# Optimization experiments

Measured on AMD Instinct MI355X. Metric: run time of the kernel, lower is better.

The kernel has to match this reference:

```python
import jax, jax.numpy as jnp
import numpy as np

WINDOW_SIZE = 64
SHIFT_SIZE = WINDOW_SIZE // 2  # shift_windows=True
HEAD_DIM = 64
SCALE = HEAD_DIM ** (-0.5)


def _shift_mask(W):
    # static shift-window mask, computed with numpy (all shapes static)
    img_mask = np.zeros((W,), dtype=np.float32)
    cnt = 0
    for s in (slice(0, -WINDOW_SIZE), slice(-WINDOW_SIZE, -SHIFT_SIZE), slice(-SHIFT_SIZE, None)):
        img_mask[s] = cnt
        cnt += 1
    mw = img_mask.reshape(W // WINDOW_SIZE, WINDOW_SIZE)  # (num_win, ws)
    mask = mw[:, None, :] - mw[:, :, None]                # (num_win, ws, ws)
    mask = np.where(mask != 0.0, -100.0, 0.0).astype(np.float32)
    return jnp.asarray(mask)


def setup_inputs() -> dict:
    key = jax.random.key(0)
    k1, k2, k3, k4 = jax.random.split(key, 4)
    B, W, C = 32, 8192, HEAD_DIM
    return {
        "q": jax.random.normal(k1, (B, W, C), dtype=jnp.float32),
        "k": jax.random.normal(k2, (B, W, C), dtype=jnp.float32),
        "v": jax.random.normal(k3, (B, W, C), dtype=jnp.float32),
        "rel_pos_table": jax.random.normal(k4, (2 * WINDOW_SIZE - 1, 1), dtype=jnp.float32) * 0.02,
    }


def reference(q, k, v, rel_pos_table):
    B, W, C = q.shape
    ws = WINDOW_SIZE
    # relative position bias gather: (1, ws, ws)
    coords = jnp.arange(ws)
    rel_idx = coords[None, :] * 0 + (coords[:, None] - coords[None, :]) + (ws - 1)  # (ws, ws)
    bias = rel_pos_table[rel_idx.reshape(-1)].reshape(ws, ws, -1)
    bias = jnp.transpose(bias, (2, 0, 1))  # (1, ws, ws)

    mask = _shift_mask(W)  # (num_win, ws, ws)

    # cyclic shift
    q = jnp.roll(q, shift=-SHIFT_SIZE, axis=1)
    k = jnp.roll(k, shift=-SHIFT_SIZE, axis=1)
    v = jnp.roll(v, shift=-SHIFT_SIZE, axis=1)

    # window partition -> (B * num_win, ws, C)
    num_win = W // ws
    qw = q.reshape(B * num_win, ws, C)
    kw = k.reshape(B * num_win, ws, C)
    vw = v.reshape(B * num_win, ws, C)

    attn = jnp.einsum('bnc,bmc->bnm', qw, kw) * SCALE + bias  # (B*nw, ws, ws)
    attn = attn.reshape(B, num_win, ws, ws) + mask[None]
    attn = attn.reshape(-1, ws, ws)
    attn = jax.nn.softmax(attn, axis=-1)

    xw = jnp.einsum('bnm,bmc->bnc', attn, vw)  # (B*nw, ws, C)
    x = xw.reshape(B, W, C)
    x = jnp.roll(x, shift=SHIFT_SIZE, axis=1)
    return (x, attn)
```

## Files before the change

kernel.cpp:

```cpp
#include <hip/hip_runtime.h>
#include <cstdint>
#include <cstddef>

#define WS 64
#define SHIFT 32
#define WTOT 8192
#define NWIN 128
#define SCALE_F 0.125f

typedef __bf16 bf16x8 __attribute__((ext_vector_type(8)));
typedef float f32x4 __attribute__((ext_vector_type(4)));

__device__ __forceinline__ unsigned short f2bf(float f) {
  unsigned int u = __builtin_bit_cast(unsigned int, f);
  u += 0x7FFFu + ((u >> 16) & 1u);
  return (unsigned short)(u >> 16);
}
__device__ __forceinline__ float bf2f(unsigned short h) {
  unsigned int u = ((unsigned int)h) << 16;
  return __builtin_bit_cast(float, u);
}

__global__ __launch_bounds__(256, 3) void win_attn(
    const float* __restrict__ q, const float* __restrict__ k,
    const float* __restrict__ v, const float* __restrict__ table,
    float* __restrict__ xout, float* __restrict__ attn_out) {
  __shared__ __align__(16) unsigned short s_qhi[WS * WS];
  __shared__ __align__(16) unsigned short s_qlo[WS * WS];
  __shared__ __align__(16) unsigned short s_khi[WS * WS];
  __shared__ __align__(16) unsigned short s_klo[WS * WS];
  __shared__ __align__(16) unsigned short s_vthi[WS * WS];
  __shared__ __align__(16) unsigned short s_vtlo[WS * WS];
  __shared__ float s_bias[2 * WS - 1];

  const int t = threadIdx.x;
  const int b = blockIdx.x;
  const int batch = b >> 7;
  const int win = b & (NWIN - 1);

  if (t < 2 * WS - 1) s_bias[t] = table[t];

  {
    const int lr = t >> 2;
    const int lc = (t & 3) << 4;
    const int grow = (win * WS + lr + SHIFT) & (WTOT - 1);
    const size_t gbase = ((size_t)batch * WTOT + grow) * WS + lc;
#pragma unroll
    for (int i = 0; i < 16; i += 4) {
      const float4 qv = *(const float4*)(q + gbase + i);
      const float4 kv = *(const float4*)(k + gbase + i);
      const float4 vv = *(const float4*)(v + gbase + i);
      const float qa[4] = {qv.x, qv.y, qv.z, qv.w};
      const float ka[4] = {kv.x, kv.y, kv.z, kv.w};
      const float va[4] = {vv.x, vv.y, vv.z, vv.w};
#pragma unroll
      for (int e = 0; e < 4; ++e) {
        const int cc = lc + i + e;
        unsigned short h;
        h = f2bf(qa[e]);
        s_qhi[lr * WS + cc] = h;
        s_qlo[lr * WS + cc] = f2bf(qa[e] - bf2f(h));
        h = f2bf(ka[e]);
        s_khi[lr * WS + cc] = h;
        s_klo[lr * WS + cc] = f2bf(ka[e] - bf2f(h));
        h = f2bf(va[e]);
        s_vthi[cc * WS + lr] = h;
        s_vtlo[cc * WS + lr] = f2bf(va[e] - bf2f(h));
      }
    }
  }
  __syncthreads();

  const int lane = t & 63;
  const int wave = t >> 6;
  const int lrow = lane & 15;
  const int quad = lane >> 4;

  const f32x4 z4 = {0.f, 0.f, 0.f, 0.f};
  f32x4 acc[4] = {z4, z4, z4, z4};
#pragma unroll
  for (int kh = 0; kh < 2; ++kh) {
    const int k0 = kh * 32 + quad * 8;
    const bf16x8 ahi = *(const bf16x8*)(s_qhi + (wave * 16 + lrow) * WS + k0);
    const bf16x8 alo = *(const bf16x8*)(s_qlo + (wave * 16 + lrow) * WS + k0);
#pragma unroll
    for (int j = 0; j < 4; ++j) {
      const bf16x8 bhi = *(const bf16x8*)(s_khi + (j * 16 + lrow) * WS + k0);
      const bf16x8 blo = *(const bf16x8*)(s_klo + (j * 16 + lrow) * WS + k0);
      acc[j] = __builtin_amdgcn_mfma_f32_16x16x32_bf16(ahi, bhi, acc[j], 0, 0, 0);
      acc[j] = __builtin_amdgcn_mfma_f32_16x16x32_bf16(alo, bhi, acc[j], 0, 0, 0);
      acc[j] = __builtin_amdgcn_mfma_f32_16x16x32_bf16(ahi, blo, acc[j], 0, 0, 0);
    }
  }

  const bool masked = (win == NWIN - 1);
  float p[4][4];
#pragma unroll
  for (int reg = 0; reg < 4; ++reg) {
    const int r = wave * 16 + quad * 4 + reg;
    float val[4];
    float vmax = -1e30f;
#pragma unroll
    for (int j = 0; j < 4; ++j) {
      const int m = j * 16 + lrow;
      float s = acc[j][reg] * SCALE_F + s_bias[r - m + (WS - 1)];
      if (masked && (((r ^ m) & 32) != 0)) s -= 100.0f;
      val[j] = s;
      vmax = fmaxf(vmax, s);
    }
#pragma unroll
    for (int off = 1; off < 16; off <<= 1)
      vmax = fmaxf(vmax, __shfl_xor(vmax, off, 64));
    float sum = 0.f;
#pragma unroll
    for (int j = 0; j < 4; ++j) {
      val[j] = __expf(val[j] - vmax);
      sum += val[j];
    }
#pragma unroll
    for (int off = 1; off < 16; off <<= 1)
      sum += __shfl_xor(sum, off, 64);
    const float inv = 1.0f / sum;
#pragma unroll
    for (int j = 0; j < 4; ++j) p[reg][j] = val[j] * inv;
  }

  {
    float* arow = attn_out + (size_t)b * (WS * WS);
#pragma unroll
    for (int reg = 0; reg < 4; ++reg) {
      const int r = wave * 16 + quad * 4 + reg;
#pragma unroll
      for (int j = 0; j < 4; ++j) {
        const int m = j * 16 + lrow;
        const float pv = p[reg][j];
        arow[r * WS + m] = pv;
        const unsigned short h = f2bf(pv);
        s_qhi[r * WS + m] = h;
        s_qlo[r * WS + m] = f2bf(pv - bf2f(h));
      }
    }
  }
  __syncthreads();

  f32x4 xacc[4] = {z4, z4, z4, z4};
#pragma unroll
  for (int kh = 0; kh < 2; ++kh) {
    const int k0 = kh * 32 + quad * 8;
    const bf16x8 phi = *(const bf16x8*)(s_qhi + (wave * 16 + lrow) * WS + k0);
    const bf16x8 plo = *(const bf16x8*)(s_qlo + (wave * 16 + lrow) * WS + k0);
#pragma unroll
    for (int j = 0; j < 4; ++j) {
      const bf16x8 vhi = *(const bf16x8*)(s_vthi + (j * 16 + lrow) * WS + k0);
      const bf16x8 vlo = *(const bf16x8*)(s_vtlo + (j * 16 + lrow) * WS + k0);
      xacc[j] = __builtin_amdgcn_mfma_f32_16x16x32_bf16(phi, vhi, xacc[j], 0, 0, 0);
      xacc[j] = __builtin_amdgcn_mfma_f32_16x16x32_bf16(plo, vhi, xacc[j], 0, 0, 0);
      xacc[j] = __builtin_amdgcn_mfma_f32_16x16x32_bf16(phi, vlo, xacc[j], 0, 0, 0);
    }
  }

#pragma unroll
  for (int reg = 0; reg < 4; ++reg) {
    const int r = wave * 16 + quad * 4 + reg;
    const int gr = (win * WS + r + SHIFT) & (WTOT - 1);
    float* xrow = xout + ((size_t)batch * WTOT + gr) * WS;
#pragma unroll
    for (int j = 0; j < 4; ++j) {
      xrow[j * 16 + lrow] = xacc[j][reg];
    }
  }
}

extern "C" void kernel_launch(void* const* d_in, const int* in_sizes, int n_in,
                              void* d_out, int out_size, void* d_ws, size_t ws_size,
                              hipStream_t stream) {
  (void)in_sizes; (void)n_in; (void)out_size; (void)d_ws; (void)ws_size;
  const float* q = (const float*)d_in[0];
  const float* k = (const float*)d_in[1];
  const float* v = (const float*)d_in[2];
  const float* table = (const float*)d_in[3];
  float* xout = (float*)d_out;
  float* attn = (float*)d_out + (size_t)32 * WTOT * WS;
  win_attn<<<dim3(4096), dim3(256), 0, stream>>>(q, k, v, table, xout, attn);
}
```

Baseline: 282.6 us.

## Load Q straight to registers, swizzle LDS, reuse K buffers for P

Q fragments are now built directly from global memory into MFMA registers, so the Q shared buffers are dropped and the K buffers are reused to stage the softmax probabilities. All LDS tiles use an XOR swizzle, and V is transposed with vectorized 4-element stores, to cut bank conflicts from the old scalar transposed writes. Bias and mask values are precomputed into registers from the global table. Less LDS per block lets launch bounds rise to 5 blocks per CU, at the cost of an extra barrier and more register pressure.

```diff
diff --git a/kernel.cpp b/kernel.cpp
--- a/kernel.cpp
+++ b/kernel.cpp
@@ -9,6 +9,8 @@
 #define SCALE_F 0.125f
 
 typedef __bf16 bf16x8 __attribute__((ext_vector_type(8)));
+typedef unsigned short u16x8 __attribute__((ext_vector_type(8)));
+typedef unsigned short u16x4 __attribute__((ext_vector_type(4)));
 typedef float f32x4 __attribute__((ext_vector_type(4)));
 
 __device__ __forceinline__ unsigned short f2bf(float f) {
@@ -21,90 +23,144 @@
   return __builtin_bit_cast(float, u);
 }
 
-__global__ __launch_bounds__(256, 3) void win_attn(
+__device__ __forceinline__ int swz(int row, int col) {
+  return (row * WS + col) ^ (((row >> 1) & 7) << 3);
+}
+
+__global__ __launch_bounds__(256, 5) void win_attn(
     const float* __restrict__ q, const float* __restrict__ k,
     const float* __restrict__ v, const float* __restrict__ table,
     float* __restrict__ xout, float* __restrict__ attn_out) {
-  __shared__ __align__(16) unsigned short s_qhi[WS * WS];
-  __shared__ __align__(16) unsigned short s_qlo[WS * WS];
   __shared__ __align__(16) unsigned short s_khi[WS * WS];
   __shared__ __align__(16) unsigned short s_klo[WS * WS];
   __shared__ __align__(16) unsigned short s_vthi[WS * WS];
   __shared__ __align__(16) unsigned short s_vtlo[WS * WS];
-  __shared__ float s_bias[2 * WS - 1];
 
   const int t = threadIdx.x;
   const int b = blockIdx.x;
   const int batch = b >> 7;
   const int win = b & (NWIN - 1);
-
-  if (t < 2 * WS - 1) s_bias[t] = table[t];
-
-  {
-    const int lr = t >> 2;
-    const int lc = (t & 3) << 4;
-    const int grow = (win * WS + lr + SHIFT) & (WTOT - 1);
-    const size_t gbase = ((size_t)batch * WTOT + grow) * WS + lc;
-#pragma unroll
-    for (int i = 0; i < 16; i += 4) {
-      const float4 qv = *(const float4*)(q + gbase + i);
-      const float4 kv = *(const float4*)(k + gbase + i);
-      const float4 vv = *(const float4*)(v + gbase + i);
-      const float qa[4] = {qv.x, qv.y, qv.z, qv.w};
-      const float ka[4] = {kv.x, kv.y, kv.z, kv.w};
-      const float va[4] = {vv.x, vv.y, vv.z, vv.w};
-#pragma unroll
-      for (int e = 0; e < 4; ++e) {
-        const int cc = lc + i + e;
-        unsigned short h;
-        h = f2bf(qa[e]);
-        s_qhi[lr * WS + cc] = h;
-        s_qlo[lr * WS + cc] = f2bf(qa[e] - bf2f(h));
-        h = f2bf(ka[e]);
-        s_khi[lr * WS + cc] = h;
-        s_klo[lr * WS + cc] = f2bf(ka[e] - bf2f(h));
-        h = f2bf(va[e]);
-        s_vthi[cc * WS + lr] = h;
-        s_vtlo[cc * WS + lr] = f2bf(va[e] - bf2f(h));
-      }
-    }
-  }
-  __syncthreads();
-
   const int lane = t & 63;
   const int wave = t >> 6;
   const int lrow = lane & 15;
   const int quad = lane >> 4;
 
+  {
+    const int lr = t >> 2;
+    const int lc = (t & 3) << 4;
+    const int grow = (win * WS + lr + SHIFT) & (WTOT - 1);
+    const float* kp = k + ((size_t)batch * WTOT + grow) * WS + lc;
+#pragma unroll
+    for (int s = 0; s < 2; ++s) {
+      const float4 x0 = *(const float4*)(kp + 8 * s);
+      const float4 x1 = *(const float4*)(kp + 8 * s + 4);
+      const float a[8] = {x0.x, x0.y, x0.z, x0.w, x1.x, x1.y, x1.z, x1.w};
+      u16x8 hi, lo;
+#pragma unroll
+      for (int e = 0; e < 8; ++e) {
+        const unsigned short h = f2bf(a[e]);
+        hi[e] = h;
+        lo[e] = f2bf(a[e] - bf2f(h));
+      }
+      const int idx = swz(lr, lc + 8 * s);
+      *(u16x8*)(s_khi + idx) = hi;
+      *(u16x8*)(s_klo + idx) = lo;
+    }
+  }
+
+  {
+    const int m0 = (t >> 4) << 2;
+    const int c0 = (t & 15) << 2;
+    float4 vr[4];
+#pragma unroll
+    for (int j = 0; j < 4; ++j) {
+      const int grow = (win * WS + m0 + j + SHIFT) & (WTOT - 1);
+      vr[j] = *(const float4*)(v + ((size_t)batch * WTOT + grow) * WS + c0);
+    }
+    const float vb[4][4] = {{vr[0].x, vr[0].y, vr[0].z, vr[0].w},
+                            {vr[1].x, vr[1].y, vr[1].z, vr[1].w},
+                            {vr[2].x, vr[2].y, vr[2].z, vr[2].w},
+                            {vr[3].x, vr[3].y, vr[3].z, vr[3].w}};
+#pragma unroll
+    for (int e = 0; e < 4; ++e) {
+      u16x4 hi, lo;
+#pragma unroll
+      for (int j = 0; j < 4; ++j) {
+        const unsigned short h = f2bf(vb[j][e]);
+        hi[j] = h;
+        lo[j] = f2bf(vb[j][e] - bf2f(h));
+      }
+      const int idx = swz(c0 + e, m0);
+      *(u16x4*)(s_vthi + idx) = hi;
+      *(u16x4*)(s_vtlo + idx) = lo;
+    }
+  }
+
+  bf16x8 qfhi[2], qflo[2];
+  {
+    const int grow = (win * WS + wave * 16 + lrow + SHIFT) & (WTOT - 1);
+    const float* qp = q + ((size_t)batch * WTOT + grow) * WS + quad * 8;
+#pragma unroll
+    for (int kh = 0; kh < 2; ++kh) {
+      const float4 x0 = *(const float4*)(qp + kh * 32);
+      const float4 x1 = *(const float4*)(qp + kh * 32 + 4);
+      const float a[8] = {x0.x, x0.y, x0.z, x0.w, x1.x, x1.y, x1.z, x1.w};
+      u16x8 hi, lo;
+#pragma unroll
+      for (int e = 0; e < 8; ++e) {
+        const unsigned short h = f2bf(a[e]);
+        hi[e] = h;
+        lo[e] = f2bf(a[e] - bf2f(h));
+      }
+      qfhi[kh] = __builtin_bit_cast(bf16x8, hi);
+      qflo[kh] = __builtin_bit_cast(bf16x8, lo);
+    }
+  }
+
+  float biasr[4][4];
+  {
+    const bool masked = (win == NWIN - 1);
+    const float* tb = table + (WS - 1);
+#pragma unroll
+    for (int reg = 0; reg < 4; ++reg) {
+      const int r = wave * 16 + quad * 4 + reg;
+#pragma unroll
+      for (int j = 0; j < 4; ++j) {
+        const int m = j * 16 + lrow;
+        float bv = __ldg(tb + (r - m));
+        if (masked && (((r ^ m) & 32) != 0)) bv -= 100.0f;
+        biasr[reg][j] = bv;
+      }
+    }
+  }
+  __syncthreads();
+
   const f32x4 z4 = {0.f, 0.f, 0.f, 0.f};
   f32x4 acc[4] = {z4, z4, z4, z4};
 #pragma unroll
   for (int kh = 0; kh < 2; ++kh) {
     const int k0 = kh * 32 + quad * 8;
-    const bf16x8 ahi = *(const bf16x8*)(s_qhi + (wave * 16 + lrow) * WS + k0);
-    const bf16x8 alo = *(const bf16x8*)(s_qlo + (wave * 16 + lrow) * WS + k0);
-#pragma unroll
-    for (int j = 0; j < 4; ++j) {
-      const bf16x8 bhi = *(const bf16x8*)(s_khi + (j * 16 + lrow) * WS + k0);
-      const bf16x8 blo = *(const bf16x8*)(s_klo + (j * 16 + lrow) * WS + k0);
+    const bf16x8 ahi = qfhi[kh];
+    const bf16x8 alo = qflo[kh];
+#pragma unroll
+    for (int j = 0; j < 4; ++j) {
+      const int idx = swz(j * 16 + lrow, k0);
+      const bf16x8 bhi = *(const bf16x8*)(s_khi + idx);
+      const bf16x8 blo = *(const bf16x8*)(s_klo + idx);
       acc[j] = __builtin_amdgcn_mfma_f32_16x16x32_bf16(ahi, bhi, acc[j], 0, 0, 0);
       acc[j] = __builtin_amdgcn_mfma_f32_16x16x32_bf16(alo, bhi, acc[j], 0, 0, 0);
       acc[j] = __builtin_amdgcn_mfma_f32_16x16x32_bf16(ahi, blo, acc[j], 0, 0, 0);
     }
   }
 
-  const bool masked = (win == NWIN - 1);
   float p[4][4];
 #pragma unroll
   for (int reg = 0; reg < 4; ++reg) {
-    const int r = wave * 16 + quad * 4 + reg;
     float val[4];
     float vmax = -1e30f;
 #pragma unroll
     for (int j = 0; j < 4; ++j) {
-      const int m = j * 16 + lrow;
-      float s = acc[j][reg] * SCALE_F + s_bias[r - m + (WS - 1)];
-      if (masked && (((r ^ m) & 32) != 0)) s -= 100.0f;
+      const float s = acc[j][reg] * SCALE_F + biasr[reg][j];
       val[j] = s;
       vmax = fmaxf(vmax, s);
     }
@@ -124,6 +180,8 @@
 #pragma unroll
     for (int j = 0; j < 4; ++j) p[reg][j] = val[j] * inv;
   }
+
+  __syncthreads();
 
   {
     float* arow = attn_out + (size_t)b * (WS * WS);
@@ -136,8 +194,9 @@
         const float pv = p[reg][j];
         arow[r * WS + m] = pv;
         const unsigned short h = f2bf(pv);
-        s_qhi[r * WS + m] = h;
-        s_qlo[r * WS + m] = f2bf(pv - bf2f(h));
+        const int idx = swz(r, m);
+        s_khi[idx] = h;
+        s_klo[idx] = f2bf(pv - bf2f(h));
       }
     }
   }
@@ -147,12 +206,14 @@
 #pragma unroll
   for (int kh = 0; kh < 2; ++kh) {
     const int k0 = kh * 32 + quad * 8;
-    const bf16x8 phi = *(const bf16x8*)(s_qhi + (wave * 16 + lrow) * WS + k0);
-    const bf16x8 plo = *(const bf16x8*)(s_qlo + (wave * 16 + lrow) * WS + k0);
-#pragma unroll
-    for (int j = 0; j < 4; ++j) {
-      const bf16x8 vhi = *(const bf16x8*)(s_vthi + (j * 16 + lrow) * WS + k0);
-      const bf16x8 vlo = *(const bf16x8*)(s_vtlo + (j * 16 + lrow) * WS + k0);
+    const int aidx = swz(wave * 16 + lrow, k0);
+    const bf16x8 phi = *(const bf16x8*)(s_khi + aidx);
+    const bf16x8 plo = *(const bf16x8*)(s_klo + aidx);
+#pragma unroll
+    for (int j = 0; j < 4; ++j) {
+      const int idx = swz(j * 16 + lrow, k0);
+      const bf16x8 vhi = *(const bf16x8*)(s_vthi + idx);
+      const bf16x8 vlo = *(const bf16x8*)(s_vtlo + idx);
       xacc[j] = __builtin_amdgcn_mfma_f32_16x16x32_bf16(phi, vhi, xacc[j], 0, 0, 0);
       xacc[j] = __builtin_amdgcn_mfma_f32_16x16x32_bf16(plo, vhi, xacc[j], 0, 0, 0);
       xacc[j] = __builtin_amdgcn_mfma_f32_16x16x32_bf16(phi, vlo, xacc[j], 0, 0, 0);
```

Measured after the change: 280.4 us. About the same (-0.8%).
